# Performance work log

Hardware: AMD Instinct MI355X
Metric: run time of the kernel (lower is better)

## Reference

```python
import jax, jax.numpy as jnp
import numpy as np

B, S, D, H = 4, 2048, 1024, 16
DH = D // H
THETA = 10000.0
STD = (2.0 / (D + D)) ** 0.5


def _rope(x):
    # x: [..., S, DH]; positions are arange(S). Rotate interleaved pairs.
    half = DH // 2
    inv_freq = THETA ** (-jnp.arange(half, dtype=jnp.float32) * 2.0 / DH)  # [half]
    ang = jnp.arange(S, dtype=jnp.float32)[:, None] * inv_freq[None, :]   # [S, half]
    cos, sin = jnp.cos(ang), jnp.sin(ang)
    x1, x2 = x[..., 0::2], x[..., 1::2]
    o1 = x1 * cos - x2 * sin
    o2 = x1 * sin + x2 * cos
    return jnp.stack([o1, o2], axis=-1).reshape(x.shape)


def setup_inputs() -> dict:
    key = jax.random.key(0)
    kx, kq, kk, kv, ko = jax.random.split(key, 5)
    return {
        "x": jax.random.normal(kx, (B, S, D), dtype=jnp.float32),
        "wq": jax.random.normal(kq, (D, D), dtype=jnp.float32) * STD,
        "wk": jax.random.normal(kk, (D, D), dtype=jnp.float32) * STD,
        "wv": jax.random.normal(kv, (D, D), dtype=jnp.float32) * STD,
        "wo": jax.random.normal(ko, (D, D), dtype=jnp.float32) * STD,
    }


def reference(x, wq, wk, wv, wo):
    # fused QKV projection (Linear with no bias: x @ W.T)
    wqkv = jnp.concatenate([wq, wk, wv], axis=0)          # [3D, D]
    qkv = jnp.einsum('bsd,ed->bse', x, wqkv)              # [B, S, 3D]
    q, k, v = jnp.split(qkv, 3, axis=-1)
    # [B, H, S, DH]
    q = q.reshape(B, S, H, DH).transpose(0, 2, 1, 3)
    k = k.reshape(B, S, H, DH).transpose(0, 2, 1, 3)
    v = v.reshape(B, S, H, DH).transpose(0, 2, 1, 3)
    q = _rope(q)
    k = _rope(k)
    scale = 1.0 / jnp.sqrt(jnp.asarray(DH, dtype=q.dtype))
    scores = jnp.einsum('bhqd,bhkd->bhqk', q, k) * scale  # [B, H, S, S]
    causal = jnp.tril(jnp.ones((S, S), dtype=bool))
    scores = jnp.where(causal, scores, -jnp.inf)
    attn = jax.nn.softmax(scores, axis=-1)
    out = jnp.einsum('bhqk,bhkd->bhqd', attn, v)          # [B, H, S, DH]
    out = out.transpose(0, 2, 1, 3).reshape(B, S, D)
    return jnp.einsum('bsd,ed->bse', out, wo)             # output proj
```

## Files before the change

kernel.cpp:

```cpp
#include <hip/hip_runtime.h>
#include <cmath>


#define S_LEN 2048
#define NHEAD 16
#define DHEAD 64

typedef short bf16x8 __attribute__((ext_vector_type(8)));
typedef float f32x4  __attribute__((ext_vector_type(4)));

__device__ __forceinline__ float bf2f(unsigned short u) {
    unsigned x = ((unsigned)u) << 16;
    return __builtin_bit_cast(float, x);
}
__device__ __forceinline__ unsigned short f2bf(float f) {
    unsigned u = __builtin_bit_cast(unsigned, f);
    unsigned r = u + 0x7fff + ((u >> 16) & 1);
    return (unsigned short)(r >> 16);
}
__device__ __forceinline__ unsigned pack2(float lo, float hi) {
    return (unsigned)f2bf(lo) | ((unsigned)f2bf(hi) << 16);
}
__device__ __forceinline__ void gl16(const void* g, void* l) {
    __builtin_amdgcn_global_load_lds(
        (const __attribute__((address_space(1))) unsigned int*)g,
        (__attribute__((address_space(3))) unsigned int*)l, 16, 0, 0);
}

__global__ void cast_f32_bf16(const float* __restrict__ in,
                              unsigned* __restrict__ out, int n)
{
    const int i = (blockIdx.x * 256 + threadIdx.x) * 8;
    if (i >= n) return;
    const float4 a = *(const float4*)(in + i);
    const float4 b = *(const float4*)(in + i + 4);
    uint4 o;
    o.x = pack2(a.x, a.y); o.y = pack2(a.z, a.w);
    o.z = pack2(b.x, b.y); o.w = pack2(b.z, b.w);
    *(uint4*)(out + i / 2) = o;
}

__global__ void cast_w4(const float* __restrict__ wq, const float* __restrict__ wk,
                        const float* __restrict__ wv, const float* __restrict__ wo,
                        unsigned* __restrict__ Wb, unsigned* __restrict__ Wob)
{
    const int idx = blockIdx.x * 256 + threadIdx.x;
    const int sel = idx >> 17;
    const int loc = idx & 131071;
    const float* src = (sel == 0) ? wq : (sel == 1) ? wk : (sel == 2) ? wv : wo;
    unsigned* dst = (sel == 3) ? Wob : Wb + (size_t)sel * 524288;
    const int i = loc * 8;
    const float4 a = *(const float4*)(src + i);
    const float4 b = *(const float4*)(src + i + 4);
    uint4 o;
    o.x = pack2(a.x, a.y); o.y = pack2(a.z, a.w);
    o.z = pack2(b.x, b.y); o.w = pack2(b.z, b.w);
    *(uint4*)(dst + i / 2) = o;
}

template <int MODE>
__global__ __launch_bounds__(256, 2) void gemm_bt(
    const unsigned short* __restrict__ A,
    const unsigned short* __restrict__ Bw,
    unsigned short* __restrict__ Qb,
    unsigned short* __restrict__ Kb,
    unsigned short* __restrict__ Vt,
    float* __restrict__ Co)
{
    __shared__ __align__(16) unsigned short As[128 * 32];
    __shared__ __align__(16) unsigned short Bs[128 * 32];

    const int t    = threadIdx.x;
    const int bm   = blockIdx.x * 128;
    const int bn   = blockIdx.y * 128;
    const int lane = t & 63, wv = t >> 6;
    const int wr   = wv >> 1, wc = wv & 1;
    const int ln   = lane & 15, ko = lane >> 4;

    f32x4 acc[4][4];
    #pragma unroll
    for (int i = 0; i < 4; ++i)
        #pragma unroll
        for (int j = 0; j < 4; ++j)
            acc[i][j] = f32x4{0.f, 0.f, 0.f, 0.f};

    const int ar  = t >> 2;
    const int asg = t & 3;
    const unsigned short* aptr = A  + (size_t)(bm + ar) * 1024 + asg * 8;
    const unsigned short* bptr = Bw + (size_t)(bn + ar) * 1024 + asg * 8;

    for (int k0 = 0; k0 < 1024; k0 += 32) {
        __syncthreads();
        gl16(aptr + k0,               (char*)As + t * 16);
        gl16(aptr + k0 + 64 * 1024,   (char*)As + (t + 256) * 16);
        gl16(bptr + k0,               (char*)Bs + t * 16);
        gl16(bptr + k0 + 64 * 1024,   (char*)Bs + (t + 256) * 16);
        __syncthreads();

        bf16x8 af[4], bfr[4];
        #pragma unroll
        for (int i = 0; i < 4; ++i)
            af[i] = *(const bf16x8*)((const char*)As + (wr * 64 + i * 16 + ln) * 64 + ko * 16);
        #pragma unroll
        for (int j = 0; j < 4; ++j)
            bfr[j] = *(const bf16x8*)((const char*)Bs + (wc * 64 + j * 16 + ln) * 64 + ko * 16);
        #pragma unroll
        for (int i = 0; i < 4; ++i)
            #pragma unroll
            for (int j = 0; j < 4; ++j)
                acc[i][j] = __builtin_amdgcn_mfma_f32_16x16x32_bf16(af[i], bfr[j], acc[i][j], 0, 0, 0);
    }

    #pragma unroll
    for (int i = 0; i < 4; ++i) {
        const int mb = bm + wr * 64 + i * 16 + ko * 4;
        #pragma unroll
        for (int j = 0; j < 4; ++j) {
            const int n = bn + wc * 64 + j * 16 + ln;
            if constexpr (MODE == 0) {
                const int which = n >> 10, nh = n & 1023;
                const int h = nh >> 6, dh = nh & 63;
                const int bb = mb >> 11, s = mb & 2047;
                const int bh = bb * NHEAD + h;
                if (which == 2) {
                    uint2 pk;
                    pk.x = pack2(acc[i][j][0], acc[i][j][1]);
                    pk.y = pack2(acc[i][j][2], acc[i][j][3]);
                    *(uint2*)&Vt[((size_t)bh * 64 + dh) * 2048 + s] = pk;
                } else {
                    unsigned short* dst = which ? Kb : Qb;
                    #pragma unroll
                    for (int r = 0; r < 4; ++r)
                        dst[((size_t)bh * 2048 + (s + r)) * 64 + dh] = f2bf(acc[i][j][r]);
                }
            } else {
                #pragma unroll
                for (int r = 0; r < 4; ++r)
                    Co[(size_t)(mb + r) * 1024 + n] = acc[i][j][r];
            }
        }
    }
}

__global__ void rope_kernel(unsigned int* __restrict__ Qb, unsigned int* __restrict__ Kb)
{
    const int idx  = blockIdx.x * 256 + threadIdx.x;
    const int i    = idx & 31;
    const int srow = (idx >> 5) & 2047;

    const float inv = powf(10000.0f, -(float)i * (1.0f / 32.0f));
    const float ang = (float)srow * inv;
    float sn, cs;
    sincosf(ang, &sn, &cs);

    const unsigned q = Qb[idx];
    const unsigned k = Kb[idx];
    const float qx = bf2f((unsigned short)(q & 0xffff)), qy = bf2f((unsigned short)(q >> 16));
    const float kx = bf2f((unsigned short)(k & 0xffff)), ky = bf2f((unsigned short)(k >> 16));
    Qb[idx] = pack2(qx * cs - qy * sn, qx * sn + qy * cs);
    Kb[idx] = pack2(kx * cs - ky * sn, kx * sn + ky * cs);
}

__device__ __forceinline__ void process_tile(
    const char* __restrict__ Ks, const char* __restrict__ Vs, char* pb,
    const bf16x8 qf[2], f32x4 ao[4], float& m_i, float& l_i,
    int ln, int koct, int qrow, bool diag)
{
    f32x4 sv[4];
    #pragma unroll
    for (int nf = 0; nf < 4; ++nf) sv[nf] = f32x4{0.f, 0.f, 0.f, 0.f};
    #pragma unroll
    for (int s = 0; s < 2; ++s) {
        #pragma unroll
        for (int nf = 0; nf < 4; ++nf) {
            const int key = nf * 16 + ln;
            const bf16x8 kf = *(const bf16x8*)(Ks + key * 128 + (((s * 4 + koct) ^ (key & 7)) * 16));
            sv[nf] = __builtin_amdgcn_mfma_f32_16x16x32_bf16(kf, qf[s], sv[nf], 0, 0, 0);
        }
    }

    if (diag) {
        #pragma unroll
        for (int nf = 0; nf < 4; ++nf) {
            #pragma unroll
            for (int r = 0; r < 4; ++r)
                if (nf * 16 + koct * 4 + r > qrow) sv[nf][r] = -INFINITY;
        }
    }

    float mx = sv[0][0];
    #pragma unroll
    for (int nf = 0; nf < 4; ++nf)
        #pragma unroll
        for (int r = 0; r < 4; ++r) mx = fmaxf(mx, sv[nf][r]);
    mx = fmaxf(mx, __shfl_xor(mx, 16));
    mx = fmaxf(mx, __shfl_xor(mx, 32));
    const float mn = fmaxf(m_i, mx);
    const float al = __expf(m_i - mn);
    m_i = mn;
    float sum = 0.f;
    #pragma unroll
    for (int nf = 0; nf < 4; ++nf)
        #pragma unroll
        for (int r = 0; r < 4; ++r) {
            const float pv = __expf(sv[nf][r] - mn);
            sv[nf][r] = pv;
            sum += pv;
        }
    sum += __shfl_xor(sum, 16);
    sum += __shfl_xor(sum, 32);
    l_i = l_i * al + sum;

    float alr[4];
    #pragma unroll
    for (int r = 0; r < 4; ++r) alr[r] = __shfl(al, koct * 4 + r);
    #pragma unroll
    for (int nf = 0; nf < 4; ++nf)
        #pragma unroll
        for (int r = 0; r < 4; ++r)
            ao[nf][r] *= alr[r];

    #pragma unroll
    for (int nf = 0; nf < 4; ++nf) {
        uint2 pk;
        pk.x = pack2(sv[nf][0], sv[nf][1]);
        pk.y = pack2(sv[nf][2], sv[nf][3]);
        *(uint2*)(pb + ln * 128 + ((nf * 32 + koct * 8) ^ ((ln & 7) << 4))) = pk;
    }

    #pragma unroll
    for (int s2 = 0; s2 < 2; ++s2) {
        const bf16x8 pa = *(const bf16x8*)(pb + ln * 128 + (((s2 * 4 + koct) ^ (ln & 7)) * 16));
        #pragma unroll
        for (int nf = 0; nf < 4; ++nf) {
            const int dh = nf * 16 + ln;
            const bf16x8 vf = *(const bf16x8*)(Vs + dh * 128 + (((s2 * 4 + koct) ^ (dh & 7)) * 16));
            ao[nf] = __builtin_amdgcn_mfma_f32_16x16x32_bf16(pa, vf, ao[nf], 0, 0, 0);
        }
    }
}

__global__ __launch_bounds__(256, 3) void attn_mfma(
    const unsigned short* __restrict__ Qb,
    const unsigned short* __restrict__ Kb,
    const unsigned short* __restrict__ Vt,
    unsigned short* __restrict__ Aot)
{
    __shared__ __align__(16) unsigned short Ksh[2][64 * 64];
    __shared__ __align__(16) unsigned short Vsh[2][64 * 64];
    __shared__ __align__(16) unsigned short Psh[4 * 16 * 64];

    const int t    = threadIdx.x;
    const int lane = t & 63, w = t >> 6;
    const int ln   = lane & 15, koct = lane >> 4;
    const int bid  = blockIdx.x;
    const int qtA  = (bid >> 3) & 15;
    const int qtB  = 31 - qtA;
    const int bh   = (bid & 7) + 8 * (bid >> 7);
    const int rA   = qtA * 64, rB = qtB * 64;
    const size_t kvbase = (size_t)bh * S_LEN * DHEAD;
    const size_t vtbase = (size_t)bh * DHEAD * S_LEN;

    bf16x8 qfA[2], qfB[2];
    #pragma unroll
    for (int s = 0; s < 2; ++s) {
        bf16x8 va = *(const bf16x8*)(Qb + kvbase + (size_t)(rA + w * 16 + ln) * 64 + s * 32 + koct * 8);
        bf16x8 vb = *(const bf16x8*)(Qb + kvbase + (size_t)(rB + w * 16 + ln) * 64 + s * 32 + koct * 8);
        #pragma unroll
        for (int j = 0; j < 8; ++j) {
            va[j] = (short)f2bf(bf2f((unsigned short)va[j]) * 0.125f);
            vb[j] = (short)f2bf(bf2f((unsigned short)vb[j]) * 0.125f);
        }
        qfA[s] = va; qfB[s] = vb;
    }

    f32x4 aoA[4], aoB[4];
    float mA = -INFINITY, lA = 0.f, mB = -INFINITY, lB = 0.f;
    #pragma unroll
    for (int nf = 0; nf < 4; ++nf) { aoA[nf] = f32x4{0.f,0.f,0.f,0.f}; aoB[nf] = f32x4{0.f,0.f,0.f,0.f}; }

    const int kr = t >> 3;
    const int sg = t & 7;
    const int kr2 = kr + 32;
    const int qrow = w * 16 + ln;

    gl16(Kb + kvbase + (size_t)kr  * 64 + (sg ^ (kr  & 7)) * 8, (char*)&Ksh[0][0] + t * 16);
    gl16(Kb + kvbase + (size_t)kr2 * 64 + (sg ^ (kr2 & 7)) * 8, (char*)&Ksh[0][0] + (t + 256) * 16);
    gl16(Vt + vtbase + (size_t)kr  * S_LEN + (sg ^ (kr  & 7)) * 8, (char*)&Vsh[0][0] + t * 16);
    gl16(Vt + vtbase + (size_t)kr2 * S_LEN + (sg ^ (kr2 & 7)) * 8, (char*)&Vsh[0][0] + (t + 256) * 16);
    __syncthreads();

    char* pb = (char*)Psh + w * 2048;
    int cur = 0;

    for (int kt = 0; kt <= qtB; ++kt) {
        if (kt < qtB) {
            const int c1 = (kt + 1) * 64;
            gl16(Kb + kvbase + (size_t)(c1 + kr)  * 64 + (sg ^ (kr  & 7)) * 8, (char*)&Ksh[cur ^ 1][0] + t * 16);
            gl16(Kb + kvbase + (size_t)(c1 + kr2) * 64 + (sg ^ (kr2 & 7)) * 8, (char*)&Ksh[cur ^ 1][0] + (t + 256) * 16);
            gl16(Vt + vtbase + (size_t)kr  * S_LEN + c1 + (sg ^ (kr  & 7)) * 8, (char*)&Vsh[cur ^ 1][0] + t * 16);
            gl16(Vt + vtbase + (size_t)kr2 * S_LEN + c1 + (sg ^ (kr2 & 7)) * 8, (char*)&Vsh[cur ^ 1][0] + (t + 256) * 16);
        }

        const char* Ks = (const char*)&Ksh[cur][0];
        const char* Vs = (const char*)&Vsh[cur][0];

        process_tile(Ks, Vs, pb, qfB, aoB, mB, lB, ln, koct, qrow, kt == qtB);
        if (kt <= qtA)
            process_tile(Ks, Vs, pb, qfA, aoA, mA, lA, ln, koct, qrow, kt == qtA);

        __syncthreads();
        cur ^= 1;
    }

    const int b = bh >> 4, h = bh & 15;
    float lAr[4], lBr[4];
    #pragma unroll
    for (int r = 0; r < 4; ++r) {
        lAr[r] = __shfl(lA, koct * 4 + r);
        lBr[r] = __shfl(lB, koct * 4 + r);
    }
    #pragma unroll
    for (int r = 0; r < 4; ++r) {
        const float invA = 1.0f / lAr[r];
        const float invB = 1.0f / lBr[r];
        const int sA = rA + w * 16 + koct * 4 + r;
        const int sB = rB + w * 16 + koct * 4 + r;
        #pragma unroll
        for (int nf = 0; nf < 4; ++nf) {
            Aot[(size_t)(b * S_LEN + sA) * 1024 + h * 64 + nf * 16 + ln] = f2bf(aoA[nf][r] * invA);
            Aot[(size_t)(b * S_LEN + sB) * 1024 + h * 64 + nf * 16 + ln] = f2bf(aoB[nf][r] * invB);
        }
    }
}

extern "C" void kernel_launch(void* const* d_in, const int* in_sizes, int n_in,
                              void* d_out, int out_size, void* d_ws, size_t ws_size,
                              hipStream_t stream)
{
    const float* x  = (const float*)d_in[0];
    const float* wq = (const float*)d_in[1];
    const float* wk = (const float*)d_in[2];
    const float* wv = (const float*)d_in[3];
    const float* wo = (const float*)d_in[4];
    float* out = (float*)d_out;

    char* p = (char*)d_ws;
    unsigned short* Xb  = (unsigned short*)p;
    unsigned short* Wb  = (unsigned short*)(p + ((size_t)16 << 20));
    unsigned short* Wob = (unsigned short*)(p + ((size_t)22 << 20));
    unsigned short* Qb  = (unsigned short*)(p + ((size_t)24 << 20));
    unsigned short* Kb  = (unsigned short*)(p + ((size_t)40 << 20));
    unsigned short* Vt  = (unsigned short*)(p + ((size_t)56 << 20));
    unsigned short* Aot = (unsigned short*)(p + ((size_t)72 << 20));

    const int NX = 8192 * 1024;
    cast_f32_bf16<<<NX / 2048, 256, 0, stream>>>(x, (unsigned*)Xb, NX);
    cast_w4<<<2048, 256, 0, stream>>>(wq, wk, wv, wo, (unsigned*)Wb, (unsigned*)Wob);

    gemm_bt<0><<<dim3(64, 24), 256, 0, stream>>>(Xb, Wb, Qb, Kb, Vt, nullptr);
    rope_kernel<<<16384, 256, 0, stream>>>((unsigned int*)Qb, (unsigned int*)Kb);
    attn_mfma<<<1024, 256, 0, stream>>>(Qb, Kb, Vt, Aot);
    gemm_bt<1><<<dim3(64, 8), 256, 0, stream>>>(Aot, Wob, nullptr, nullptr, nullptr, out);
}
```

Before: 293.3 us.

## Process four query tiles per attention block, lazy rescale, BK=64 swizzled GEMM

The attention kernel now has each block handle four causally balanced query tiles of one head instead of two. Each K/V tile loaded into shared memory is therefore reused four times, and the grid shrinks to 512 blocks with occupancy lowered to 2. Online softmax skips the rescale of the running max and accumulators unless the new max exceeds the old one by more than 8, which removes exp and shuffle work on most tiles. The GEMM doubles its K-tile to 64 using an XOR-swizzled LDS layout to cut barriers and bank conflicts. The trade-offs are more register pressure and fewer blocks in flight, which may hurt latency hiding.

```diff
diff --git a/kernel.cpp b/kernel.cpp
--- a/kernel.cpp
+++ b/kernel.cpp
@@ -67,8 +67,8 @@
     unsigned short* __restrict__ Vt,
     float* __restrict__ Co)
 {
-    __shared__ __align__(16) unsigned short As[128 * 32];
-    __shared__ __align__(16) unsigned short Bs[128 * 32];
+    __shared__ __align__(16) unsigned short As[128 * 64];
+    __shared__ __align__(16) unsigned short Bs[128 * 64];
 
     const int t    = threadIdx.x;
     const int bm   = blockIdx.x * 128;
@@ -84,31 +84,39 @@
         for (int j = 0; j < 4; ++j)
             acc[i][j] = f32x4{0.f, 0.f, 0.f, 0.f};
 
-    const int ar  = t >> 2;
-    const int asg = t & 3;
-    const unsigned short* aptr = A  + (size_t)(bm + ar) * 1024 + asg * 8;
-    const unsigned short* bptr = Bw + (size_t)(bn + ar) * 1024 + asg * 8;
-
-    for (int k0 = 0; k0 < 1024; k0 += 32) {
+    const int sr  = t >> 3;
+    const int sg  = t & 7;
+    const int swz = (sg ^ (sr & 7)) * 8;
+    const unsigned short* aptr = A  + (size_t)(bm + sr) * 1024 + swz;
+    const unsigned short* bptr = Bw + (size_t)(bn + sr) * 1024 + swz;
+
+    for (int k0 = 0; k0 < 1024; k0 += 64) {
         __syncthreads();
-        gl16(aptr + k0,               (char*)As + t * 16);
-        gl16(aptr + k0 + 64 * 1024,   (char*)As + (t + 256) * 16);
-        gl16(bptr + k0,               (char*)Bs + t * 16);
-        gl16(bptr + k0 + 64 * 1024,   (char*)Bs + (t + 256) * 16);
+        #pragma unroll
+        for (int i = 0; i < 4; ++i) {
+            gl16(aptr + k0 + i * 32 * 1024, (char*)As + t * 16 + i * 4096);
+            gl16(bptr + k0 + i * 32 * 1024, (char*)Bs + t * 16 + i * 4096);
+        }
         __syncthreads();
 
-        bf16x8 af[4], bfr[4];
-        #pragma unroll
-        for (int i = 0; i < 4; ++i)
-            af[i] = *(const bf16x8*)((const char*)As + (wr * 64 + i * 16 + ln) * 64 + ko * 16);
-        #pragma unroll
-        for (int j = 0; j < 4; ++j)
-            bfr[j] = *(const bf16x8*)((const char*)Bs + (wc * 64 + j * 16 + ln) * 64 + ko * 16);
-        #pragma unroll
-        for (int i = 0; i < 4; ++i)
+        #pragma unroll
+        for (int s = 0; s < 2; ++s) {
+            bf16x8 af[4], bfr[4];
+            #pragma unroll
+            for (int i = 0; i < 4; ++i)
+                af[i] = *(const bf16x8*)((const char*)As +
+                         (wr * 64 + i * 16 + ln) * 128 + (((s * 4 + ko) ^ (ln & 7)) * 16));
             #pragma unroll
             for (int j = 0; j < 4; ++j)
-                acc[i][j] = __builtin_amdgcn_mfma_f32_16x16x32_bf16(af[i], bfr[j], acc[i][j], 0, 0, 0);
+                bfr[j] = *(const bf16x8*)((const char*)Bs +
+                         (wc * 64 + j * 16 + ln) * 128 + (((s * 4 + ko) ^ (ln & 7)) * 16));
+            #pragma unroll
+            for (int i = 0; i < 4; ++i)
+                #pragma unroll
+                for (int j = 0; j < 4; ++j)
+                    acc[i][j] = __builtin_amdgcn_mfma_f32_16x16x32_bf16(
+                        af[i], bfr[j], acc[i][j], 0, 0, 0);
+        }
     }
 
     #pragma unroll
@@ -195,30 +203,34 @@
         for (int r = 0; r < 4; ++r) mx = fmaxf(mx, sv[nf][r]);
     mx = fmaxf(mx, __shfl_xor(mx, 16));
     mx = fmaxf(mx, __shfl_xor(mx, 32));
-    const float mn = fmaxf(m_i, mx);
-    const float al = __expf(m_i - mn);
-    m_i = mn;
+
+    if (!__all(mx <= m_i + 8.0f)) {
+        const float mn = fmaxf(m_i, mx);
+        const float al = __expf(m_i - mn);
+        m_i = mn;
+        l_i *= al;
+        float alr[4];
+        #pragma unroll
+        for (int r = 0; r < 4; ++r) alr[r] = __shfl(al, koct * 4 + r);
+        #pragma unroll
+        for (int nf = 0; nf < 4; ++nf)
+            #pragma unroll
+            for (int r = 0; r < 4; ++r)
+                ao[nf][r] *= alr[r];
+    }
+
     float sum = 0.f;
     #pragma unroll
     for (int nf = 0; nf < 4; ++nf)
         #pragma unroll
         for (int r = 0; r < 4; ++r) {
-            const float pv = __expf(sv[nf][r] - mn);
+            const float pv = __expf(sv[nf][r] - m_i);
             sv[nf][r] = pv;
             sum += pv;
         }
     sum += __shfl_xor(sum, 16);
     sum += __shfl_xor(sum, 32);
-    l_i = l_i * al + sum;
-
-    float alr[4];
-    #pragma unroll
-    for (int r = 0; r < 4; ++r) alr[r] = __shfl(al, koct * 4 + r);
-    #pragma unroll
-    for (int nf = 0; nf < 4; ++nf)
-        #pragma unroll
-        for (int r = 0; r < 4; ++r)
-            ao[nf][r] *= alr[r];
+    l_i += sum;
 
     #pragma unroll
     for (int nf = 0; nf < 4; ++nf) {
@@ -240,7 +252,7 @@
     }
 }
 
-__global__ __launch_bounds__(256, 3) void attn_mfma(
+__global__ __launch_bounds__(256, 2) void attn_mfma(
     const unsigned short* __restrict__ Qb,
     const unsigned short* __restrict__ Kb,
     const unsigned short* __restrict__ Vt,
@@ -254,35 +266,42 @@
     const int lane = t & 63, w = t >> 6;
     const int ln   = lane & 15, koct = lane >> 4;
     const int bid  = blockIdx.x;
-    const int qtA  = (bid >> 3) & 15;
-    const int qtB  = 31 - qtA;
-    const int bh   = (bid & 7) + 8 * (bid >> 7);
-    const int rA   = qtA * 64, rB = qtB * 64;
+    const int xcd  = bid & 7;
+    const int i2   = bid >> 3;
+    const int bh   = xcd + 8 * (i2 & 7);
+    const int j    = i2 >> 3;
+    const int qts[4] = {31 - j, 23 - j, j + 8, j};
     const size_t kvbase = (size_t)bh * S_LEN * DHEAD;
     const size_t vtbase = (size_t)bh * DHEAD * S_LEN;
 
-    bf16x8 qfA[2], qfB[2];
-    #pragma unroll
-    for (int s = 0; s < 2; ++s) {
-        bf16x8 va = *(const bf16x8*)(Qb + kvbase + (size_t)(rA + w * 16 + ln) * 64 + s * 32 + koct * 8);
-        bf16x8 vb = *(const bf16x8*)(Qb + kvbase + (size_t)(rB + w * 16 + ln) * 64 + s * 32 + koct * 8);
-        #pragma unroll
-        for (int j = 0; j < 8; ++j) {
-            va[j] = (short)f2bf(bf2f((unsigned short)va[j]) * 0.125f);
-            vb[j] = (short)f2bf(bf2f((unsigned short)vb[j]) * 0.125f);
-        }
-        qfA[s] = va; qfB[s] = vb;
-    }
-
-    f32x4 aoA[4], aoB[4];
-    float mA = -INFINITY, lA = 0.f, mB = -INFINITY, lB = 0.f;
-    #pragma unroll
-    for (int nf = 0; nf < 4; ++nf) { aoA[nf] = f32x4{0.f,0.f,0.f,0.f}; aoB[nf] = f32x4{0.f,0.f,0.f,0.f}; }
+    bf16x8 qf[4][2];
+    #pragma unroll
+    for (int u = 0; u < 4; ++u) {
+        #pragma unroll
+        for (int s = 0; s < 2; ++s) {
+            bf16x8 v = *(const bf16x8*)(Qb + kvbase +
+                (size_t)(qts[u] * 64 + w * 16 + ln) * 64 + s * 32 + koct * 8);
+            #pragma unroll
+            for (int e = 0; e < 8; ++e)
+                v[e] = (short)f2bf(bf2f((unsigned short)v[e]) * 0.125f);
+            qf[u][s] = v;
+        }
+    }
+
+    f32x4 ao[4][4];
+    float m_i[4], l_i[4];
+    #pragma unroll
+    for (int u = 0; u < 4; ++u) {
+        m_i[u] = -INFINITY; l_i[u] = 0.f;
+        #pragma unroll
+        for (int nf = 0; nf < 4; ++nf) ao[u][nf] = f32x4{0.f, 0.f, 0.f, 0.f};
+    }
 
     const int kr = t >> 3;
     const int sg = t & 7;
     const int kr2 = kr + 32;
     const int qrow = w * 16 + ln;
+    const int ktmax = qts[0];
 
     gl16(Kb + kvbase + (size_t)kr  * 64 + (sg ^ (kr  & 7)) * 8, (char*)&Ksh[0][0] + t * 16);
     gl16(Kb + kvbase + (size_t)kr2 * 64 + (sg ^ (kr2 & 7)) * 8, (char*)&Ksh[0][0] + (t + 256) * 16);
@@ -293,8 +312,8 @@
     char* pb = (char*)Psh + w * 2048;
     int cur = 0;
 
-    for (int kt = 0; kt <= qtB; ++kt) {
-        if (kt < qtB) {
+    for (int kt = 0; kt <= ktmax; ++kt) {
+        if (kt < ktmax) {
             const int c1 = (kt + 1) * 64;
             gl16(Kb + kvbase + (size_t)(c1 + kr)  * 64 + (sg ^ (kr  & 7)) * 8, (char*)&Ksh[cur ^ 1][0] + t * 16);
             gl16(Kb + kvbase + (size_t)(c1 + kr2) * 64 + (sg ^ (kr2 & 7)) * 8, (char*)&Ksh[cur ^ 1][0] + (t + 256) * 16);
@@ -305,31 +324,32 @@
         const char* Ks = (const char*)&Ksh[cur][0];
         const char* Vs = (const char*)&Vsh[cur][0];
 
-        process_tile(Ks, Vs, pb, qfB, aoB, mB, lB, ln, koct, qrow, kt == qtB);
-        if (kt <= qtA)
-            process_tile(Ks, Vs, pb, qfA, aoA, mA, lA, ln, koct, qrow, kt == qtA);
+        process_tile(Ks, Vs, pb, qf[0], ao[0], m_i[0], l_i[0], ln, koct, qrow, kt == qts[0]);
+        if (kt <= qts[1])
+            process_tile(Ks, Vs, pb, qf[1], ao[1], m_i[1], l_i[1], ln, koct, qrow, kt == qts[1]);
+        if (kt <= qts[2])
+            process_tile(Ks, Vs, pb, qf[2], ao[2], m_i[2], l_i[2], ln, koct, qrow, kt == qts[2]);
+        if (kt <= qts[3])
+            process_tile(Ks, Vs, pb, qf[3], ao[3], m_i[3], l_i[3], ln, koct, qrow, kt == qts[3]);
 
         __syncthreads();
         cur ^= 1;
     }
 
     const int b = bh >> 4, h = bh & 15;
-    float lAr[4], lBr[4];
-    #pragma unroll
-    for (int r = 0; r < 4; ++r) {
-        lAr[r] = __shfl(lA, koct * 4 + r);
-        lBr[r] = __shfl(lB, koct * 4 + r);
-    }
-    #pragma unroll
-    for (int r = 0; r < 4; ++r) {
-        const float invA = 1.0f / lAr[r];
-        const float invB = 1.0f / lBr[r];
-        const int sA = rA + w * 16 + koct * 4 + r;
-        const int sB = rB + w * 16 + koct * 4 + r;
-        #pragma unroll
-        for (int nf = 0; nf < 4; ++nf) {
-            Aot[(size_t)(b * S_LEN + sA) * 1024 + h * 64 + nf * 16 + ln] = f2bf(aoA[nf][r] * invA);
-            Aot[(size_t)(b * S_LEN + sB) * 1024 + h * 64 + nf * 16 + ln] = f2bf(aoB[nf][r] * invB);
+    #pragma unroll
+    for (int u = 0; u < 4; ++u) {
+        float lr[4];
+        #pragma unroll
+        for (int r = 0; r < 4; ++r) lr[r] = __shfl(l_i[u], koct * 4 + r);
+        #pragma unroll
+        for (int r = 0; r < 4; ++r) {
+            const float inv = 1.0f / lr[r];
+            const int s = qts[u] * 64 + w * 16 + koct * 4 + r;
+            #pragma unroll
+            for (int nf = 0; nf < 4; ++nf)
+                Aot[(size_t)(b * S_LEN + s) * 1024 + h * 64 + nf * 16 + ln] =
+                    f2bf(ao[u][nf][r] * inv);
         }
     }
 }
@@ -360,6 +380,6 @@
 
     gemm_bt<0><<<dim3(64, 24), 256, 0, stream>>>(Xb, Wb, Qb, Kb, Vt, nullptr);
     rope_kernel<<<16384, 256, 0, stream>>>((unsigned int*)Qb, (unsigned int*)Kb);
-    attn_mfma<<<1024, 256, 0, stream>>>(Qb, Kb, Vt, Aot);
+    attn_mfma<<<512, 256, 0, stream>>>(Qb, Kb, Vt, Aot);
     gemm_bt<1><<<dim3(64, 8), 256, 0, stream>>>(Aot, Wob, nullptr, nullptr, nullptr, out);
 }
```

Result: faster. 257.8 us (-12.1%).
